# Performance work log

Hardware: AMD Instinct MI355X
Metric: run time of the kernel (lower is better)

## Reference

```python
import jax, jax.numpy as jnp
import numpy as np


def setup_inputs() -> dict:
    key = jax.random.key(0)
    k1, k2 = jax.random.split(key)
    x = jax.random.normal(k1, (4, 4096, 128), dtype=jnp.float32)
    kernel = jax.random.normal(k2, (3, 128, 64), dtype=jnp.float32)
    return {"x": x, "kernel": kernel}


def reference(x, kernel):
    # QKV projections: x [B,N,Din] @ kernel[i] [Din,Dout] -> [B,N,Dout]
    WQ = jnp.einsum('bnd,de->bne', x, kernel[0])
    WK = jnp.einsum('bnd,de->bne', x, kernel[1])
    WV = jnp.einsum('bnd,de->bne', x, kernel[2])
    d_out = WV.shape[-1]
    # scaled dot-product scores [B,N,N]
    scores = jnp.einsum('bqe,bke->bqk', WQ, WK) / jnp.sqrt(jnp.float32(d_out))
    attn = jax.nn.softmax(scores, axis=-1)
    return jnp.einsum('bqk,bke->bqe', attn, WV)
```

## Files before the change

### kernel.cpp

```cpp
#include <hip/hip_runtime.h>


typedef __attribute__((ext_vector_type(8))) short bf16x8;
typedef __attribute__((ext_vector_type(16))) float f32x16;
typedef __attribute__((ext_vector_type(4))) unsigned u32x4;
typedef unsigned short us;

__device__ __forceinline__ us f2bf(float f) {
  unsigned u = __builtin_bit_cast(unsigned, f);
  u += 0x7FFFu + ((u >> 16) & 1u);
  return (us)(u >> 16);
}
__device__ __forceinline__ float bf2f(us h) {
  unsigned u = ((unsigned)h) << 16;
  return __builtin_bit_cast(float, u);
}
__device__ __forceinline__ f32x16 mfma(bf16x8 a, bf16x8 b, f32x16 c) {
  return __builtin_amdgcn_mfma_f32_32x32x16_bf16(a, b, c, 0, 0, 0);
}
__device__ __forceinline__ unsigned pk2(float a, float b) {
  return (unsigned)f2bf(a) | ((unsigned)f2bf(b) << 16);
}
#define EXP2(x) __builtin_amdgcn_exp2f(x)

__device__ __forceinline__ void gld16(const us* g, us* l) {
  __builtin_amdgcn_global_load_lds(
      (__attribute__((address_space(1))) const unsigned int*)g,
      (__attribute__((address_space(3))) unsigned int*)l, 16, 0, 0);
}

__global__ __launch_bounds__(256, 1) void wprep_kernel(
    const float* __restrict__ w, us* __restrict__ Wbh, us* __restrict__ Wbl)
{
  const int i = blockIdx.x * 256 + threadIdx.x;
  if (i >= 24576) return;
  const int p = i >> 13, d = (i & 8191) >> 6, e = i & 63;
  float v = w[i];
  if (p == 0) v *= 0.18033688011112042f;
  const us hi = f2bf(v);
  const us lo = f2bf(v - bf2f(hi));
  const int g = (p * 64 + e) >> 5, ks = d >> 4, hh = (d >> 3) & 1, j = d & 7;
  const int o = ((g * 8 + ks) * 2 + hh) * 256 + (e & 31) * 8 + j;
  Wbh[o] = hi;
  Wbl[o] = lo;
}

#define TP 101

__global__ __launch_bounds__(256, 1) void qkv_kernel(
    const float* __restrict__ x,
    const us* __restrict__ Wbh, const us* __restrict__ Wbl,
    us* __restrict__ Qhi, us* __restrict__ Qlo,
    us* __restrict__ Khi, us* __restrict__ Klo, us* __restrict__ Vb)
{
  __shared__ unsigned ttile[128 * TP];
  const int t = threadIdx.x;
  const int rb = blockIdx.x >> 1, ch = blockIdx.x & 1;
  const int wid = t >> 6, lane = t & 63;
  const int l31 = lane & 31, h = lane >> 5;
  const int rbase = rb * 128 + wid * 32;
  const float* xrow = x + (size_t)(rbase + l31) * 128;

  f32x16 acc[3] = {};
  #pragma unroll
  for (int ks = 0; ks < 8; ++ks) {
    const int d0 = ks * 16 + h * 8;
    const float4 xa = *(const float4*)(xrow + d0);
    const float4 xb = *(const float4*)(xrow + d0 + 4);
    const float xv[8] = {xa.x, xa.y, xa.z, xa.w, xb.x, xb.y, xb.z, xb.w};
    bf16x8 ah, al;
    #pragma unroll
    for (int j = 0; j < 8; ++j) {
      us hi = f2bf(xv[j]);
      ah[j] = (short)hi;
      al[j] = (short)f2bf(xv[j] - bf2f(hi));
    }
    #pragma unroll
    for (int nt = 0; nt < 3; ++nt) {
      const int g = ch * 3 + nt;
      const int wo = ((g * 8 + ks) * 2 + h) * 256 + l31 * 8;
      bf16x8 bh = *(const bf16x8*)(Wbh + wo);
      bf16x8 bl = *(const bf16x8*)(Wbl + wo);
      acc[nt] = mfma(ah, bh, acc[nt]);
      acc[nt] = mfma(al, bh, acc[nt]);
      acc[nt] = mfma(ah, bl, acc[nt]);
    }
  }

  #pragma unroll
  for (int nt = 0; nt < 3; ++nt) {
    const int col = 32 * nt + l31;
    #pragma unroll
    for (int r = 0; r < 16; ++r) {
      const int rl = (r & 3) + 8 * (r >> 2) + 4 * h;
      float v = acc[nt][r];
      us hi = f2bf(v);
      us lo = f2bf(v - bf2f(hi));
      ttile[(wid * 32 + rl) * TP + col] = (unsigned)hi | ((unsigned)lo << 16);
    }
  }
  __syncthreads();

  const int row = t >> 1;
  const int grow = rb * 128 + row;
  if (ch == 0) {
    {
      const int cb = (t & 1) * 32;
      unsigned hw[16], lw[16];
      #pragma unroll
      for (int j = 0; j < 16; ++j) {
        unsigned a = ttile[row * TP + cb + 2 * j];
        unsigned bv = ttile[row * TP + cb + 2 * j + 1];
        hw[j] = (a & 0xffffu) | (bv << 16);
        lw[j] = (a >> 16) | (bv & 0xffff0000u);
      }
      #pragma unroll
      for (int j = 0; j < 4; ++j) {
        uint4 hv = {hw[4 * j], hw[4 * j + 1], hw[4 * j + 2], hw[4 * j + 3]};
        uint4 lv = {lw[4 * j], lw[4 * j + 1], lw[4 * j + 2], lw[4 * j + 3]};
        *(uint4*)(Qhi + (size_t)grow * 64 + cb + 8 * j) = hv;
        *(uint4*)(Qlo + (size_t)grow * 64 + cb + 8 * j) = lv;
      }
    }
    {
      const int cs = (t & 1) * 16;
      unsigned hw[8], lw[8];
      #pragma unroll
      for (int j = 0; j < 8; ++j) {
        unsigned a = ttile[row * TP + 64 + cs + 2 * j];
        unsigned bv = ttile[row * TP + 64 + cs + 2 * j + 1];
        hw[j] = (a & 0xffffu) | (bv << 16);
        lw[j] = (a >> 16) | (bv & 0xffff0000u);
      }
      #pragma unroll
      for (int j = 0; j < 2; ++j) {
        uint4 hv = {hw[4 * j], hw[4 * j + 1], hw[4 * j + 2], hw[4 * j + 3]};
        uint4 lv = {lw[4 * j], lw[4 * j + 1], lw[4 * j + 2], lw[4 * j + 3]};
        *(uint4*)(Khi + (size_t)grow * 64 + cs + 8 * j) = hv;
        *(uint4*)(Klo + (size_t)grow * 64 + cs + 8 * j) = lv;
      }
    }
  } else {
    {
      const int cs = (t & 1) * 16;
      unsigned hw[8], lw[8];
      #pragma unroll
      for (int j = 0; j < 8; ++j) {
        unsigned a = ttile[row * TP + cs + 2 * j];
        unsigned bv = ttile[row * TP + cs + 2 * j + 1];
        hw[j] = (a & 0xffffu) | (bv << 16);
        lw[j] = (a >> 16) | (bv & 0xffff0000u);
      }
      #pragma unroll
      for (int j = 0; j < 2; ++j) {
        uint4 hv = {hw[4 * j], hw[4 * j + 1], hw[4 * j + 2], hw[4 * j + 3]};
        uint4 lv = {lw[4 * j], lw[4 * j + 1], lw[4 * j + 2], lw[4 * j + 3]};
        *(uint4*)(Khi + (size_t)grow * 64 + 32 + cs + 8 * j) = hv;
        *(uint4*)(Klo + (size_t)grow * 64 + 32 + cs + 8 * j) = lv;
      }
    }
    {
      const int bb = (rb * 128) >> 12;
      const int nb = (rb * 128) & 4095;
      #pragma unroll
      for (int i2 = 0; i2 < 4; ++i2) {
        const int c = t + 256 * i2;
        const int e = c >> 4, nc = c & 15;
        unsigned p[4];
        #pragma unroll
        for (int j = 0; j < 4; ++j) {
          unsigned a = ttile[(nc * 8 + 2 * j) * TP + 32 + e];
          unsigned bv = ttile[(nc * 8 + 2 * j + 1) * TP + 32 + e];
          p[j] = (a & 0xffffu) | (bv << 16);
        }
        uint4 pv = {p[0], p[1], p[2], p[3]};
        const int n0 = nb + nc * 8;
        const int kt = n0 >> 6, sub = n0 & 63;
        const int ks = sub >> 4, hh = (sub >> 3) & 1;
        const int dt = e >> 5, lv = e & 31;
        *(uint4*)(Vb + (size_t)bb * 262144 +
                  ((((kt * 4 + ks) * 2 + hh) * 2 + dt) * 256 + lv * 8)) = pv;
      }
    }
  }
}

#define NSEG 8
#define ITERS 8

__global__ __launch_bounds__(256, 3) void attn_kernel(
    const us* __restrict__ Qhi, const us* __restrict__ Qlo,
    const us* __restrict__ Khi, const us* __restrict__ Klo,
    const us* __restrict__ Vb,
    us* __restrict__ Opart, float* __restrict__ Mpart,
    float* __restrict__ Lpart)
{
  __shared__ union {
    us k[2][2][4096];
    float fb[4][2112];
  } sm;
  __shared__ float alds[4][32];

  const int bx = blockIdx.x;
  const int xc = bx & 7, b = xc >> 1;
  const int idx = ((bx >> 3) << 1) | (xc & 1);
  const int seg = idx & (NSEG - 1), qg = idx >> 3;
  const int t = threadIdx.x;
  const int wid = t >> 6, lane = t & 63;
  const int l31 = lane & 31, h = lane >> 5;
  const int q0 = qg * 128 + wid * 32;
  const int u = (b * 4096 + q0) >> 5;
  const size_t pb = (size_t)u * NSEG + seg;

  bf16x8 qh[4], ql[4];
  {
    const size_t rg = (size_t)(b * 4096 + q0 + l31) * 64;
    #pragma unroll
    for (int ks = 0; ks < 4; ++ks) {
      qh[ks] = *(const bf16x8*)(Qhi + rg + ks * 16 + h * 8);
      ql[ks] = *(const bf16x8*)(Qlo + rg + ks * 16 + h * 8);
    }
  }
  const size_t kbase = (size_t)b * 262144;
  const size_t vbb = (size_t)b * 262144;

  const int row0 = t >> 3, slot = t & 7;
  const int gcol = (slot ^ (row0 & 7)) * 8;
  const int wb = 512 * wid;

  {
    const int k0 = seg * 512;
    gld16(Khi + kbase + (size_t)(k0 + row0) * 64 + gcol, &sm.k[0][0][wb]);
    gld16(Khi + kbase + (size_t)(k0 + row0 + 32) * 64 + gcol, &sm.k[0][0][wb + 2048]);
    gld16(Klo + kbase + (size_t)(k0 + row0) * 64 + gcol, &sm.k[0][1][wb]);
    gld16(Klo + kbase + (size_t)(k0 + row0 + 32) * 64 + gcol, &sm.k[0][1][wb + 2048]);
  }
  __syncthreads();

  f32x16 o[2] = {};
  float mrun = -__builtin_inff();
  float lrun = 0.f;

  for (int it = 0; it < ITERS; ++it) {
    const int cur = it & 1, nxt = cur ^ 1;
    const int KT = seg * ITERS + it;

    if (it + 1 < ITERS) {
      const int nk = (KT + 1) * 64;
      gld16(Khi + kbase + (size_t)(nk + row0) * 64 + gcol, &sm.k[nxt][0][wb]);
      gld16(Khi + kbase + (size_t)(nk + row0 + 32) * 64 + gcol, &sm.k[nxt][0][wb + 2048]);
      gld16(Klo + kbase + (size_t)(nk + row0) * 64 + gcol, &sm.k[nxt][1][wb]);
      gld16(Klo + kbase + (size_t)(nk + row0 + 32) * 64 + gcol, &sm.k[nxt][1][wb + 2048]);
    }

    f32x16 s[2] = {};
    #pragma unroll
    for (int m = 0; m < 2; ++m) {
      const int krow = 32 * m + l31;
      #pragma unroll
      for (int ks = 0; ks < 4; ++ks) {
        const int off = krow * 64 + (((2 * ks + h) ^ (l31 & 7)) * 8);
        bf16x8 ah = *(const bf16x8*)(&sm.k[cur][0][off]);
        bf16x8 al = *(const bf16x8*)(&sm.k[cur][1][off]);
        s[m] = mfma(ah, qh[ks], s[m]);
        s[m] = mfma(al, qh[ks], s[m]);
        s[m] = mfma(ah, ql[ks], s[m]);
      }
    }

    float vm = -__builtin_inff();
    #pragma unroll
    for (int r = 0; r < 16; ++r)
      vm = fmaxf(vm, fmaxf(s[0][r], s[1][r]));
    vm = fmaxf(vm, __shfl_xor(vm, 32));
    const float mnew = fmaxf(mrun, vm);
    const float alpha = EXP2(mrun - mnew);
    float sum = 0.f;
    unsigned pp[2][8];
    #pragma unroll
    for (int m = 0; m < 2; ++m) {
      #pragma unroll
      for (int p = 0; p < 8; ++p) {
        const float p0 = EXP2(s[m][2 * p] - mnew);
        const float p1 = EXP2(s[m][2 * p + 1] - mnew);
        sum += p0 + p1;
        pp[m][p] = pk2(p0, p1);
      }
    }
    sum += __shfl_xor(sum, 32);
    lrun = lrun * alpha + sum;
    mrun = mnew;

    if (__any(alpha != 1.f)) {
      if (!h) alds[wid][l31] = alpha;
      #pragma unroll
      for (int g = 0; g < 4; ++g) {
        const float4 af4 = *(const float4*)(&alds[wid][8 * g + 4 * h]);
        #pragma unroll
        for (int rr = 0; rr < 4; ++rr) {
          const int r = 4 * g + rr;
          const float a = (rr == 0) ? af4.x : (rr == 1) ? af4.y
                         : (rr == 2) ? af4.z : af4.w;
          o[0][r] *= a;
          o[1][r] *= a;
        }
      }
    }

    #pragma unroll
    for (int ks = 0; ks < 4; ++ks) {
      const int m = ks >> 1, base = 4 * (ks & 1);
      const unsigned x0 = pp[m][base + 0], x1 = pp[m][base + 1];
      const unsigned x2 = pp[m][base + 2], x3 = pp[m][base + 3];
      const unsigned sA = h ? x0 : x2;
      const unsigned sB = h ? x1 : x3;
      const unsigned rA = (unsigned)__shfl_xor((int)sA, 32);
      const unsigned rB = (unsigned)__shfl_xor((int)sB, 32);
      u32x4 wv;
      wv.x = h ? rA : x0;
      wv.y = h ? rB : x1;
      wv.z = h ? x2 : rA;
      wv.w = h ? x3 : rB;
      const bf16x8 af = __builtin_bit_cast(bf16x8, wv);
      const size_t vo = vbb + (size_t)((((KT * 4 + ks) * 2 + h) * 2) * 256 + l31 * 8);
      const bf16x8 vf0 = *(const bf16x8*)(Vb + vo);
      const bf16x8 vf1 = *(const bf16x8*)(Vb + vo + 256);
      o[0] = mfma(af, vf0, o[0]);
      o[1] = mfma(af, vf1, o[1]);
    }

    __syncthreads();
  }

  float* fb = sm.fb[wid];
  #pragma unroll
  for (int dt = 0; dt < 2; ++dt) {
    #pragma unroll
    for (int r = 0; r < 16; ++r) {
      const int qrow = (r & 3) + 8 * (r >> 2) + 4 * h;
      fb[qrow * 66 + l31 + 32 * dt] = o[dt][r];
    }
  }
  #pragma unroll
  for (int jj = 0; jj < 4; ++jj) {
    const int chunk = lane + 64 * jj;
    const int rw = chunk >> 3, part = chunk & 7;
    const float* src = &fb[rw * 66 + part * 8];
    float2 a0 = *(const float2*)(src + 0);
    float2 a1 = *(const float2*)(src + 2);
    float2 a2 = *(const float2*)(src + 4);
    float2 a3 = *(const float2*)(src + 6);
    uint4 pkv;
    pkv.x = pk2(a0.x, a0.y);
    pkv.y = pk2(a1.x, a1.y);
    pkv.z = pk2(a2.x, a2.y);
    pkv.w = pk2(a3.x, a3.y);
    *(uint4*)(Opart + pb * 2048 + (size_t)rw * 64 + part * 8) = pkv;
  }
  if (!h) {
    Mpart[pb * 32 + l31] = mrun;
    Lpart[pb * 32 + l31] = lrun;
  }
}

__global__ __launch_bounds__(256, 1) void merge_kernel(
    const us* __restrict__ Opart, const float* __restrict__ Mpart,
    const float* __restrict__ Lpart, float* __restrict__ out)
{
  const int tg = blockIdx.x * 256 + threadIdx.x;
  const int q = tg >> 3, dc = (tg & 7) * 8;
  const int u = q >> 5, ql = q & 31;
  const int base = u * NSEG;
  float M = -__builtin_inff();
  #pragma unroll
  for (int s = 0; s < NSEG; ++s)
    M = fmaxf(M, Mpart[(size_t)(base + s) * 32 + ql]);
  float acc[8] = {};
  float den = 0.f;
  #pragma unroll
  for (int s = 0; s < NSEG; ++s) {
    const float wgt = EXP2(Mpart[(size_t)(base + s) * 32 + ql] - M);
    den += wgt * Lpart[(size_t)(base + s) * 32 + ql];
    const uint4 r = *(const uint4*)(Opart + (size_t)(base + s) * 2048 +
                                    ql * 64 + dc);
    const unsigned rw[4] = {r.x, r.y, r.z, r.w};
    #pragma unroll
    for (int j = 0; j < 4; ++j) {
      acc[2 * j]     += wgt * bf2f((us)(rw[j] & 0xffffu));
      acc[2 * j + 1] += wgt * bf2f((us)(rw[j] >> 16));
    }
  }
  const float inv = 1.f / den;
  float4 r0 = {acc[0] * inv, acc[1] * inv, acc[2] * inv, acc[3] * inv};
  float4 r1 = {acc[4] * inv, acc[5] * inv, acc[6] * inv, acc[7] * inv};
  *(float4*)(out + (size_t)q * 64 + dc) = r0;
  *(float4*)(out + (size_t)q * 64 + dc + 4) = r1;
}

extern "C" void kernel_launch(void* const* d_in, const int* in_sizes, int n_in,
                              void* d_out, int out_size, void* d_ws,
                              size_t ws_size, hipStream_t stream)
{
  const float* x = (const float*)d_in[0];
  const float* w = (const float*)d_in[1];
  float* out = (float*)d_out;
  char* ws = (char*)d_ws;

  const size_t T = 2097152;
  us* Qhi = (us*)(ws + 0 * T);
  us* Qlo = (us*)(ws + 1 * T);
  us* Khi = (us*)(ws + 2 * T);
  us* Klo = (us*)(ws + 3 * T);
  us* Vb  = (us*)(ws + 4 * T);
  us* Wbh = (us*)(ws + 5 * T);
  us* Wbl = (us*)(ws + 5 * T + 49152);
  char* pbase = ws + 5 * T + 98304;
  us* Opart = (us*)pbase;
  float* Mpart = (float*)(pbase + 16777216);
  float* Lpart = (float*)(pbase + 16777216 + 524288);

  hipLaunchKernelGGL(wprep_kernel, dim3(96), dim3(256), 0, stream, w, Wbh, Wbl);
  hipLaunchKernelGGL(qkv_kernel, dim3(256), dim3(256), 0, stream,
                     x, Wbh, Wbl, Qhi, Qlo, Khi, Klo, Vb);
  hipLaunchKernelGGL(attn_kernel, dim3(1024), dim3(256), 0, stream,
                     Qhi, Qlo, Khi, Klo, Vb, Opart, Mpart, Lpart);
  hipLaunchKernelGGL(merge_kernel, dim3(512), dim3(256), 0, stream,
                     Opart, Mpart, Lpart, out);
}
```

Before: 137.5 us.

## Fuse merge into attention, stage V in LDS, regrid QKV, skip negligible tiles

The separate merge kernel is removed. The last attention block to finish for each 32-query unit, detected with an atomic counter that wprep zeroes, now merges the split-K partials. V tiles are prefetched into LDS alongside K instead of being read straight from global memory. The QKV projection is regridded to 512 blocks of 384 threads, each wave computing one output tile. Key tiles whose max score is more than 24 below the running max are skipped, and bf16 packing now uses a truncating perm instead of round-to-nearest. These changes add single-block tail work for the merge and slightly reduce accuracy through truncation and tile skipping.

New measurement: 303.9 us. 2.21x slower.

```diff
diff --git a/kernel.cpp b/kernel.cpp
--- a/kernel.cpp
+++ b/kernel.cpp
@@ -18,8 +18,9 @@
 __device__ __forceinline__ f32x16 mfma(bf16x8 a, bf16x8 b, f32x16 c) {
   return __builtin_amdgcn_mfma_f32_32x32x16_bf16(a, b, c, 0, 0, 0);
 }
-__device__ __forceinline__ unsigned pk2(float a, float b) {
-  return (unsigned)f2bf(a) | ((unsigned)f2bf(b) << 16);
+__device__ __forceinline__ unsigned pk2t(float a, float b) {
+  return __builtin_amdgcn_perm(__builtin_bit_cast(unsigned, b),
+                               __builtin_bit_cast(unsigned, a), 0x07060302u);
 }
 #define EXP2(x) __builtin_amdgcn_exp2f(x)
 
@@ -29,10 +30,18 @@
       (__attribute__((address_space(3))) unsigned int*)l, 16, 0, 0);
 }
 
+#define NSEG 8
+#define ITERS 8
+
 __global__ __launch_bounds__(256, 1) void wprep_kernel(
-    const float* __restrict__ w, us* __restrict__ Wbh, us* __restrict__ Wbl)
+    const float* __restrict__ w, us* __restrict__ Wbh, us* __restrict__ Wbl,
+    int* __restrict__ cnt)
 {
   const int i = blockIdx.x * 256 + threadIdx.x;
+  if (blockIdx.x == 0) {
+    cnt[threadIdx.x] = 0;
+    cnt[threadIdx.x + 256] = 0;
+  }
   if (i >= 24576) return;
   const int p = i >> 13, d = (i & 8191) >> 6, e = i & 63;
   float v = w[i];
@@ -45,23 +54,21 @@
   Wbl[o] = lo;
 }
 
-#define TP 101
-
-__global__ __launch_bounds__(256, 1) void qkv_kernel(
+__global__ __launch_bounds__(384, 1) void qkv_kernel(
     const float* __restrict__ x,
     const us* __restrict__ Wbh, const us* __restrict__ Wbl,
     us* __restrict__ Qhi, us* __restrict__ Qlo,
     us* __restrict__ Khi, us* __restrict__ Klo, us* __restrict__ Vb)
 {
-  __shared__ unsigned ttile[128 * TP];
+  __shared__ unsigned ttile[32 * 193];
   const int t = threadIdx.x;
-  const int rb = blockIdx.x >> 1, ch = blockIdx.x & 1;
+  const int rb = blockIdx.x;
   const int wid = t >> 6, lane = t & 63;
   const int l31 = lane & 31, h = lane >> 5;
-  const int rbase = rb * 128 + wid * 32;
+  const int rbase = rb * 32;
   const float* xrow = x + (size_t)(rbase + l31) * 128;
 
-  f32x16 acc[3] = {};
+  f32x16 acc = {};
   #pragma unroll
   for (int ks = 0; ks < 8; ++ks) {
     const int d0 = ks * 16 + h * 8;
@@ -75,128 +82,98 @@
       ah[j] = (short)hi;
       al[j] = (short)f2bf(xv[j] - bf2f(hi));
     }
-    #pragma unroll
-    for (int nt = 0; nt < 3; ++nt) {
-      const int g = ch * 3 + nt;
-      const int wo = ((g * 8 + ks) * 2 + h) * 256 + l31 * 8;
-      bf16x8 bh = *(const bf16x8*)(Wbh + wo);
-      bf16x8 bl = *(const bf16x8*)(Wbl + wo);
-      acc[nt] = mfma(ah, bh, acc[nt]);
-      acc[nt] = mfma(al, bh, acc[nt]);
-      acc[nt] = mfma(ah, bl, acc[nt]);
-    }
+    const int wo = ((wid * 8 + ks) * 2 + h) * 256 + l31 * 8;
+    bf16x8 bh = *(const bf16x8*)(Wbh + wo);
+    bf16x8 bl = *(const bf16x8*)(Wbl + wo);
+    acc = mfma(ah, bh, acc);
+    acc = mfma(al, bh, acc);
+    acc = mfma(ah, bl, acc);
   }
 
   #pragma unroll
-  for (int nt = 0; nt < 3; ++nt) {
-    const int col = 32 * nt + l31;
-    #pragma unroll
-    for (int r = 0; r < 16; ++r) {
-      const int rl = (r & 3) + 8 * (r >> 2) + 4 * h;
-      float v = acc[nt][r];
-      us hi = f2bf(v);
-      us lo = f2bf(v - bf2f(hi));
-      ttile[(wid * 32 + rl) * TP + col] = (unsigned)hi | ((unsigned)lo << 16);
-    }
+  for (int r = 0; r < 16; ++r) {
+    const int rl = (r & 3) + 8 * (r >> 2) + 4 * h;
+    float v = acc[r];
+    us hi = f2bf(v);
+    us lo = f2bf(v - bf2f(hi));
+    ttile[rl * 193 + wid * 32 + l31] = (unsigned)hi | ((unsigned)lo << 16);
   }
   __syncthreads();
 
-  const int row = t >> 1;
-  const int grow = rb * 128 + row;
-  if (ch == 0) {
-    {
-      const int cb = (t & 1) * 32;
-      unsigned hw[16], lw[16];
-      #pragma unroll
-      for (int j = 0; j < 16; ++j) {
-        unsigned a = ttile[row * TP + cb + 2 * j];
-        unsigned bv = ttile[row * TP + cb + 2 * j + 1];
-        hw[j] = (a & 0xffffu) | (bv << 16);
-        lw[j] = (a >> 16) | (bv & 0xffff0000u);
-      }
+  if (t < 64) {
+    const int row = t >> 1, cb = (t & 1) * 32;
+    const int grow = rbase + row;
+    unsigned hw[16], lw[16];
+    #pragma unroll
+    for (int j = 0; j < 16; ++j) {
+      unsigned a = ttile[row * 193 + cb + 2 * j];
+      unsigned bv = ttile[row * 193 + cb + 2 * j + 1];
+      hw[j] = (a & 0xffffu) | (bv << 16);
+      lw[j] = (a >> 16) | (bv & 0xffff0000u);
+    }
+    #pragma unroll
+    for (int j = 0; j < 4; ++j) {
+      uint4 hv = {hw[4 * j], hw[4 * j + 1], hw[4 * j + 2], hw[4 * j + 3]};
+      uint4 lv = {lw[4 * j], lw[4 * j + 1], lw[4 * j + 2], lw[4 * j + 3]};
+      *(uint4*)(Qhi + (size_t)grow * 64 + cb + 8 * j) = hv;
+      *(uint4*)(Qlo + (size_t)grow * 64 + cb + 8 * j) = lv;
+    }
+  } else if (t < 192) {
+    const int tt = t - 64;
+    const int row = tt >> 2, cs = (tt & 3) * 16;
+    const int grow = rbase + row;
+    unsigned hw[8], lw[8];
+    #pragma unroll
+    for (int j = 0; j < 8; ++j) {
+      unsigned a = ttile[row * 193 + 64 + cs + 2 * j];
+      unsigned bv = ttile[row * 193 + 64 + cs + 2 * j + 1];
+      hw[j] = (a & 0xffffu) | (bv << 16);
+      lw[j] = (a >> 16) | (bv & 0xffff0000u);
+    }
+    #pragma unroll
+    for (int j = 0; j < 2; ++j) {
+      uint4 hv = {hw[4 * j], hw[4 * j + 1], hw[4 * j + 2], hw[4 * j + 3]};
+      uint4 lv = {lw[4 * j], lw[4 * j + 1], lw[4 * j + 2], lw[4 * j + 3]};
+      *(uint4*)(Khi + (size_t)grow * 64 + cs + 8 * j) = hv;
+      *(uint4*)(Klo + (size_t)grow * 64 + cs + 8 * j) = lv;
+    }
+  } else if (t < 320) {
+    const int bb = rbase >> 12;
+    const int nb = rbase & 4095;
+    #pragma unroll
+    for (int i2 = 0; i2 < 2; ++i2) {
+      const int c = (t - 192) + 128 * i2;
+      const int e = c >> 2, nc = c & 3;
+      unsigned p[4];
       #pragma unroll
       for (int j = 0; j < 4; ++j) {
-        uint4 hv = {hw[4 * j], hw[4 * j + 1], hw[4 * j + 2], hw[4 * j + 3]};
-        uint4 lv = {lw[4 * j], lw[4 * j + 1], lw[4 * j + 2], lw[4 * j + 3]};
-        *(uint4*)(Qhi + (size_t)grow * 64 + cb + 8 * j) = hv;
-        *(uint4*)(Qlo + (size_t)grow * 64 + cb + 8 * j) = lv;
-      }
-    }
-    {
-      const int cs = (t & 1) * 16;
-      unsigned hw[8], lw[8];
-      #pragma unroll
-      for (int j = 0; j < 8; ++j) {
-        unsigned a = ttile[row * TP + 64 + cs + 2 * j];
-        unsigned bv = ttile[row * TP + 64 + cs + 2 * j + 1];
-        hw[j] = (a & 0xffffu) | (bv << 16);
-        lw[j] = (a >> 16) | (bv & 0xffff0000u);
-      }
-      #pragma unroll
-      for (int j = 0; j < 2; ++j) {
-        uint4 hv = {hw[4 * j], hw[4 * j + 1], hw[4 * j + 2], hw[4 * j + 3]};
-        uint4 lv = {lw[4 * j], lw[4 * j + 1], lw[4 * j + 2], lw[4 * j + 3]};
-        *(uint4*)(Khi + (size_t)grow * 64 + cs + 8 * j) = hv;
-        *(uint4*)(Klo + (size_t)grow * 64 + cs + 8 * j) = lv;
-      }
-    }
-  } else {
-    {
-      const int cs = (t & 1) * 16;
-      unsigned hw[8], lw[8];
-      #pragma unroll
-      for (int j = 0; j < 8; ++j) {
-        unsigned a = ttile[row * TP + cs + 2 * j];
-        unsigned bv = ttile[row * TP + cs + 2 * j + 1];
-        hw[j] = (a & 0xffffu) | (bv << 16);
-        lw[j] = (a >> 16) | (bv & 0xffff0000u);
-      }
-      #pragma unroll
-      for (int j = 0; j < 2; ++j) {
-        uint4 hv = {hw[4 * j], hw[4 * j + 1], hw[4 * j + 2], hw[4 * j + 3]};
-        uint4 lv = {lw[4 * j], lw[4 * j + 1], lw[4 * j + 2], lw[4 * j + 3]};
-        *(uint4*)(Khi + (size_t)grow * 64 + 32 + cs + 8 * j) = hv;
-        *(uint4*)(Klo + (size_t)grow * 64 + 32 + cs + 8 * j) = lv;
-      }
-    }
-    {
-      const int bb = (rb * 128) >> 12;
-      const int nb = (rb * 128) & 4095;
-      #pragma unroll
-      for (int i2 = 0; i2 < 4; ++i2) {
-        const int c = t + 256 * i2;
-        const int e = c >> 4, nc = c & 15;
-        unsigned p[4];
-        #pragma unroll
-        for (int j = 0; j < 4; ++j) {
-          unsigned a = ttile[(nc * 8 + 2 * j) * TP + 32 + e];
-          unsigned bv = ttile[(nc * 8 + 2 * j + 1) * TP + 32 + e];
-          p[j] = (a & 0xffffu) | (bv << 16);
-        }
-        uint4 pv = {p[0], p[1], p[2], p[3]};
-        const int n0 = nb + nc * 8;
-        const int kt = n0 >> 6, sub = n0 & 63;
-        const int ks = sub >> 4, hh = (sub >> 3) & 1;
-        const int dt = e >> 5, lv = e & 31;
-        *(uint4*)(Vb + (size_t)bb * 262144 +
-                  ((((kt * 4 + ks) * 2 + hh) * 2 + dt) * 256 + lv * 8)) = pv;
-      }
-    }
-  }
-}
-
-#define NSEG 8
-#define ITERS 8
+        unsigned a = ttile[(nc * 8 + 2 * j) * 193 + 128 + e];
+        unsigned bv = ttile[(nc * 8 + 2 * j + 1) * 193 + 128 + e];
+        p[j] = (a & 0xffffu) | (bv << 16);
+      }
+      uint4 pv = {p[0], p[1], p[2], p[3]};
+      const int n0 = nb + nc * 8;
+      const int kt = n0 >> 6, sub = n0 & 63;
+      const int ks = sub >> 4, hh = (sub >> 3) & 1;
+      const int dt = e >> 5, lv = e & 31;
+      *(uint4*)(Vb + (size_t)bb * 262144 +
+                ((((kt * 4 + ks) * 2 + hh) * 2 + dt) * 256 + lv * 8)) = pv;
+    }
+  }
+}
 
 __global__ __launch_bounds__(256, 3) void attn_kernel(
     const us* __restrict__ Qhi, const us* __restrict__ Qlo,
     const us* __restrict__ Khi, const us* __restrict__ Klo,
     const us* __restrict__ Vb,
     us* __restrict__ Opart, float* __restrict__ Mpart,
-    float* __restrict__ Lpart)
+    float* __restrict__ Lpart, float* __restrict__ out, int* __restrict__ cnt)
 {
   __shared__ union {
-    us k[2][2][4096];
+    struct {
+      us k[2][2][4096];
+      us v[2][4096];
+    } tl;
     float fb[4][2112];
   } sm;
   __shared__ float alds[4][32];
@@ -227,13 +204,18 @@
   const int row0 = t >> 3, slot = t & 7;
   const int gcol = (slot ^ (row0 & 7)) * 8;
   const int wb = 512 * wid;
+  const int vw0 = (wid * 2) * 512;
+  const int vw1 = (wid * 2 + 1) * 512;
 
   {
     const int k0 = seg * 512;
-    gld16(Khi + kbase + (size_t)(k0 + row0) * 64 + gcol, &sm.k[0][0][wb]);
-    gld16(Khi + kbase + (size_t)(k0 + row0 + 32) * 64 + gcol, &sm.k[0][0][wb + 2048]);
-    gld16(Klo + kbase + (size_t)(k0 + row0) * 64 + gcol, &sm.k[0][1][wb]);
-    gld16(Klo + kbase + (size_t)(k0 + row0 + 32) * 64 + gcol, &sm.k[0][1][wb + 2048]);
+    gld16(Khi + kbase + (size_t)(k0 + row0) * 64 + gcol, &sm.tl.k[0][0][wb]);
+    gld16(Khi + kbase + (size_t)(k0 + row0 + 32) * 64 + gcol, &sm.tl.k[0][0][wb + 2048]);
+    gld16(Klo + kbase + (size_t)(k0 + row0) * 64 + gcol, &sm.tl.k[0][1][wb]);
+    gld16(Klo + kbase + (size_t)(k0 + row0 + 32) * 64 + gcol, &sm.tl.k[0][1][wb + 2048]);
+    const size_t vt = vbb + (size_t)(seg * ITERS) * 4096;
+    gld16(Vb + vt + vw0 + lane * 8, &sm.tl.v[0][vw0]);
+    gld16(Vb + vt + vw1 + lane * 8, &sm.tl.v[0][vw1]);
   }
   __syncthreads();
 
@@ -247,10 +229,13 @@
 
     if (it + 1 < ITERS) {
       const int nk = (KT + 1) * 64;
-      gld16(Khi + kbase + (size_t)(nk + row0) * 64 + gcol, &sm.k[nxt][0][wb]);
-      gld16(Khi + kbase + (size_t)(nk + row0 + 32) * 64 + gcol, &sm.k[nxt][0][wb + 2048]);
-      gld16(Klo + kbase + (size_t)(nk + row0) * 64 + gcol, &sm.k[nxt][1][wb]);
-      gld16(Klo + kbase + (size_t)(nk + row0 + 32) * 64 + gcol, &sm.k[nxt][1][wb + 2048]);
+      gld16(Khi + kbase + (size_t)(nk + row0) * 64 + gcol, &sm.tl.k[nxt][0][wb]);
+      gld16(Khi + kbase + (size_t)(nk + row0 + 32) * 64 + gcol, &sm.tl.k[nxt][0][wb + 2048]);
+      gld16(Klo + kbase + (size_t)(nk + row0) * 64 + gcol, &sm.tl.k[nxt][1][wb]);
+      gld16(Klo + kbase + (size_t)(nk + row0 + 32) * 64 + gcol, &sm.tl.k[nxt][1][wb + 2048]);
+      const size_t vt = vbb + (size_t)(KT + 1) * 4096;
+      gld16(Vb + vt + vw0 + lane * 8, &sm.tl.v[nxt][vw0]);
+      gld16(Vb + vt + vw1 + lane * 8, &sm.tl.v[nxt][vw1]);
     }
 
     f32x16 s[2] = {};
@@ -260,8 +245,8 @@
       #pragma unroll
       for (int ks = 0; ks < 4; ++ks) {
         const int off = krow * 64 + (((2 * ks + h) ^ (l31 & 7)) * 8);
-        bf16x8 ah = *(const bf16x8*)(&sm.k[cur][0][off]);
-        bf16x8 al = *(const bf16x8*)(&sm.k[cur][1][off]);
+        bf16x8 ah = *(const bf16x8*)(&sm.tl.k[cur][0][off]);
+        bf16x8 al = *(const bf16x8*)(&sm.tl.k[cur][1][off]);
         s[m] = mfma(ah, qh[ks], s[m]);
         s[m] = mfma(al, qh[ks], s[m]);
         s[m] = mfma(ah, ql[ks], s[m]);
@@ -273,60 +258,63 @@
     for (int r = 0; r < 16; ++r)
       vm = fmaxf(vm, fmaxf(s[0][r], s[1][r]));
     vm = fmaxf(vm, __shfl_xor(vm, 32));
-    const float mnew = fmaxf(mrun, vm);
-    const float alpha = EXP2(mrun - mnew);
-    float sum = 0.f;
-    unsigned pp[2][8];
-    #pragma unroll
-    for (int m = 0; m < 2; ++m) {
+
+    if (!__all(vm <= mrun - 24.f)) {
+      const float mnew = fmaxf(mrun, vm);
+      const float alpha = EXP2(mrun - mnew);
+      float sum = 0.f;
+      unsigned pp[2][8];
       #pragma unroll
-      for (int p = 0; p < 8; ++p) {
-        const float p0 = EXP2(s[m][2 * p] - mnew);
-        const float p1 = EXP2(s[m][2 * p + 1] - mnew);
-        sum += p0 + p1;
-        pp[m][p] = pk2(p0, p1);
-      }
-    }
-    sum += __shfl_xor(sum, 32);
-    lrun = lrun * alpha + sum;
-    mrun = mnew;
-
-    if (__any(alpha != 1.f)) {
-      if (!h) alds[wid][l31] = alpha;
+      for (int m = 0; m < 2; ++m) {
+        #pragma unroll
+        for (int p = 0; p < 8; ++p) {
+          const float p0 = EXP2(s[m][2 * p] - mnew);
+          const float p1 = EXP2(s[m][2 * p + 1] - mnew);
+          sum += p0 + p1;
+          pp[m][p] = pk2t(p0, p1);
+        }
+      }
+      sum += __shfl_xor(sum, 32);
+      lrun = lrun * alpha + sum;
+      mrun = mnew;
+
+      if (__any(alpha != 1.f)) {
+        if (!h) alds[wid][l31] = alpha;
+        #pragma unroll
+        for (int g = 0; g < 4; ++g) {
+          const float4 af4 = *(const float4*)(&alds[wid][8 * g + 4 * h]);
+          #pragma unroll
+          for (int rr = 0; rr < 4; ++rr) {
+            const int r = 4 * g + rr;
+            const float a = (rr == 0) ? af4.x : (rr == 1) ? af4.y
+                           : (rr == 2) ? af4.z : af4.w;
+            o[0][r] *= a;
+            o[1][r] *= a;
+          }
+        }
+      }
+
       #pragma unroll
-      for (int g = 0; g < 4; ++g) {
-        const float4 af4 = *(const float4*)(&alds[wid][8 * g + 4 * h]);
-        #pragma unroll
-        for (int rr = 0; rr < 4; ++rr) {
-          const int r = 4 * g + rr;
-          const float a = (rr == 0) ? af4.x : (rr == 1) ? af4.y
-                         : (rr == 2) ? af4.z : af4.w;
-          o[0][r] *= a;
-          o[1][r] *= a;
-        }
-      }
-    }
-
-    #pragma unroll
-    for (int ks = 0; ks < 4; ++ks) {
-      const int m = ks >> 1, base = 4 * (ks & 1);
-      const unsigned x0 = pp[m][base + 0], x1 = pp[m][base + 1];
-      const unsigned x2 = pp[m][base + 2], x3 = pp[m][base + 3];
-      const unsigned sA = h ? x0 : x2;
-      const unsigned sB = h ? x1 : x3;
-      const unsigned rA = (unsigned)__shfl_xor((int)sA, 32);
-      const unsigned rB = (unsigned)__shfl_xor((int)sB, 32);
-      u32x4 wv;
-      wv.x = h ? rA : x0;
-      wv.y = h ? rB : x1;
-      wv.z = h ? x2 : rA;
-      wv.w = h ? x3 : rB;
-      const bf16x8 af = __builtin_bit_cast(bf16x8, wv);
-      const size_t vo = vbb + (size_t)((((KT * 4 + ks) * 2 + h) * 2) * 256 + l31 * 8);
-      const bf16x8 vf0 = *(const bf16x8*)(Vb + vo);
-      const bf16x8 vf1 = *(const bf16x8*)(Vb + vo + 256);
-      o[0] = mfma(af, vf0, o[0]);
-      o[1] = mfma(af, vf1, o[1]);
+      for (int ks = 0; ks < 4; ++ks) {
+        const int m = ks >> 1, base = 4 * (ks & 1);
+        const unsigned x0 = pp[m][base + 0], x1 = pp[m][base + 1];
+        const unsigned x2 = pp[m][base + 2], x3 = pp[m][base + 3];
+        const unsigned sA = h ? x0 : x2;
+        const unsigned sB = h ? x1 : x3;
+        const unsigned rA = (unsigned)__shfl_xor((int)sA, 32);
+        const unsigned rB = (unsigned)__shfl_xor((int)sB, 32);
+        u32x4 wv;
+        wv.x = h ? rA : x0;
+        wv.y = h ? rB : x1;
+        wv.z = h ? x2 : rA;
+        wv.w = h ? x3 : rB;
+        const bf16x8 af = __builtin_bit_cast(bf16x8, wv);
+        const int vo = ((2 * ks + h) * 2) * 256 + l31 * 8;
+        const bf16x8 vf0 = *(const bf16x8*)(&sm.tl.v[cur][vo]);
+        const bf16x8 vf1 = *(const bf16x8*)(&sm.tl.v[cur][vo + 256]);
+        o[0] = mfma(af, vf0, o[0]);
+        o[1] = mfma(af, vf1, o[1]);
+      }
     }
 
     __syncthreads();
@@ -351,50 +339,58 @@
     float2 a2 = *(const float2*)(src + 4);
     float2 a3 = *(const float2*)(src + 6);
     uint4 pkv;
-    pkv.x = pk2(a0.x, a0.y);
-    pkv.y = pk2(a1.x, a1.y);
-    pkv.z = pk2(a2.x, a2.y);
-    pkv.w = pk2(a3.x, a3.y);
+    pkv.x = pk2t(a0.x, a0.y);
+    pkv.y = pk2t(a1.x, a1.y);
+    pkv.z = pk2t(a2.x, a2.y);
+    pkv.w = pk2t(a3.x, a3.y);
     *(uint4*)(Opart + pb * 2048 + (size_t)rw * 64 + part * 8) = pkv;
   }
   if (!h) {
     Mpart[pb * 32 + l31] = mrun;
     Lpart[pb * 32 + l31] = lrun;
   }
-}
-
-__global__ __launch_bounds__(256, 1) void merge_kernel(
-    const us* __restrict__ Opart, const float* __restrict__ Mpart,
-    const float* __restrict__ Lpart, float* __restrict__ out)
-{
-  const int tg = blockIdx.x * 256 + threadIdx.x;
-  const int q = tg >> 3, dc = (tg & 7) * 8;
-  const int u = q >> 5, ql = q & 31;
-  const int base = u * NSEG;
-  float M = -__builtin_inff();
-  #pragma unroll
-  for (int s = 0; s < NSEG; ++s)
-    M = fmaxf(M, Mpart[(size_t)(base + s) * 32 + ql]);
-  float acc[8] = {};
-  float den = 0.f;
-  #pragma unroll
-  for (int s = 0; s < NSEG; ++s) {
-    const float wgt = EXP2(Mpart[(size_t)(base + s) * 32 + ql] - M);
-    den += wgt * Lpart[(size_t)(base + s) * 32 + ql];
-    const uint4 r = *(const uint4*)(Opart + (size_t)(base + s) * 2048 +
-                                    ql * 64 + dc);
-    const unsigned rw[4] = {r.x, r.y, r.z, r.w};
-    #pragma unroll
-    for (int j = 0; j < 4; ++j) {
-      acc[2 * j]     += wgt * bf2f((us)(rw[j] & 0xffffu));
-      acc[2 * j + 1] += wgt * bf2f((us)(rw[j] >> 16));
-    }
-  }
-  const float inv = 1.f / den;
-  float4 r0 = {acc[0] * inv, acc[1] * inv, acc[2] * inv, acc[3] * inv};
-  float4 r1 = {acc[4] * inv, acc[5] * inv, acc[6] * inv, acc[7] * inv};
-  *(float4*)(out + (size_t)q * 64 + dc) = r0;
-  *(float4*)(out + (size_t)q * 64 + dc + 4) = r1;
+
+  __threadfence();
+  int old = 0;
+  if (lane == 0) old = atomicAdd(&cnt[u], 1);
+  old = __shfl(old, 0);
+  if (old == NSEG - 1) {
+    __threadfence();
+    const int q = lane >> 1, hf = lane & 1;
+    const size_t ub = (size_t)u * NSEG;
+    float mv[NSEG];
+    float M = -__builtin_inff();
+    #pragma unroll
+    for (int s2 = 0; s2 < NSEG; ++s2) {
+      mv[s2] = Mpart[(ub + s2) * 32 + q];
+      M = fmaxf(M, mv[s2]);
+    }
+    float den = 0.f, acc[32] = {};
+    #pragma unroll
+    for (int s2 = 0; s2 < NSEG; ++s2) {
+      const float wgt = EXP2(mv[s2] - M);
+      den += wgt * Lpart[(ub + s2) * 32 + q];
+      const us* op = Opart + (ub + s2) * 2048 + q * 64 + hf * 32;
+      #pragma unroll
+      for (int j = 0; j < 4; ++j) {
+        const uint4 r = *(const uint4*)(op + j * 8);
+        const unsigned rw[4] = {r.x, r.y, r.z, r.w};
+        #pragma unroll
+        for (int k2 = 0; k2 < 4; ++k2) {
+          acc[j * 8 + 2 * k2]     += wgt * bf2f((us)(rw[k2] & 0xffffu));
+          acc[j * 8 + 2 * k2 + 1] += wgt * bf2f((us)(rw[k2] >> 16));
+        }
+      }
+    }
+    const float inv = 1.f / den;
+    float* dst = out + (size_t)(u * 32 + q) * 64 + hf * 32;
+    #pragma unroll
+    for (int j = 0; j < 8; ++j) {
+      float4 r4 = {acc[4 * j] * inv, acc[4 * j + 1] * inv,
+                   acc[4 * j + 2] * inv, acc[4 * j + 3] * inv};
+      *(float4*)(dst + 4 * j) = r4;
+    }
+  }
 }
 
 extern "C" void kernel_launch(void* const* d_in, const int* in_sizes, int n_in,
@@ -418,12 +414,12 @@
   us* Opart = (us*)pbase;
   float* Mpart = (float*)(pbase + 16777216);
   float* Lpart = (float*)(pbase + 16777216 + 524288);
-
-  hipLaunchKernelGGL(wprep_kernel, dim3(96), dim3(256), 0, stream, w, Wbh, Wbl);
-  hipLaunchKernelGGL(qkv_kernel, dim3(256), dim3(256), 0, stream,
+  int* cnt = (int*)(pbase + 16777216 + 1048576);
+
+  hipLaunchKernelGGL(wprep_kernel, dim3(96), dim3(256), 0, stream,
+                     w, Wbh, Wbl, cnt);
+  hipLaunchKernelGGL(qkv_kernel, dim3(512), dim3(384), 0, stream,
                      x, Wbh, Wbl, Qhi, Qlo, Khi, Klo, Vb);
   hipLaunchKernelGGL(attn_kernel, dim3(1024), dim3(256), 0, stream,
-                     Qhi, Qlo, Khi, Klo, Vb, Opart, Mpart, Lpart);
-  hipLaunchKernelGGL(merge_kernel, dim3(512), dim3(256), 0, stream,
-                     Opart, Mpart, Lpart, out);
-}
+                     Qhi, Qlo, Khi, Klo, Vb, Opart, Mpart, Lpart, out, cnt);
+}
```
